# Optimization experiments

Hardware: AMD Instinct MI355X
Metric: run time of the kernel (lower is better)

Reference implementation:

```python
import jax, jax.numpy as jnp
import numpy as np

RES_LIST = [16, 32, 64, 128]
N_DIMS = 3
N_FIELDS = 4
N_POINTS = 2_000_000


def _value_noise(x, V, res, mult):
    """One ValueNoise level: trilinear interpolation of grid V at points x.

    x: [N, n_dims] float, V: [(res+1),]*n_dims + [n_fields], smoothness=2.
    """
    n_dims = x.shape[1]
    xs = jnp.fmod(x * res, res)                      # [N, d]
    fl = jnp.floor(xs)
    locs = xs - fl                                   # frac part, [N, d]
    ia = fl.astype(jnp.int32)                        # floor index
    ib = ia + 1                                      # non-periodic: grid has res+1 nodes
    idx = jnp.stack((ia, ib), axis=-1)               # [N, d, 2]
    corners = jnp.indices((2,) * n_dims)             # [d, 2,2,2]
    # per-dim corner indices, each [N, 2,2,2]
    gather_idx = tuple(idx[:, i, :][:, corners[i]] for i in range(n_dims))
    vals = V[gather_idx]                             # [N, 2,2,2, n_fields]
    # smoothness=2 fade: w = (3 - 2w) w^2
    w = (3.0 - 2.0 * locs) * locs * locs             # [N, d]
    for i in range(n_dims):
        wi = w[:, i].reshape((-1,) + (1,) * (n_dims - i))
        a, b = vals[:, 0], vals[:, 1]
        vals = a + wi * (b - a)                      # lerp along dim i
    return vals * mult                               # [N, n_fields]


def setup_inputs() -> dict:
    key = jax.random.key(0)
    kx, k0, k1, k2, k3 = jax.random.split(key, 5)
    x = jax.random.uniform(kx, (N_POINTS, N_DIMS), dtype=jnp.float32)
    grids = {}
    for k, res in zip((k0, k1, k2, k3), RES_LIST):
        grids[f"V{res}"] = jax.random.normal(
            k, (res + 1,) * N_DIMS + (N_FIELDS,), dtype=jnp.float32)
    return {"x": x, **grids}


def reference(x, V16, V32, V64, V128):
    grids = (V16, V32, V64, V128)
    out = jnp.zeros((x.shape[0], N_FIELDS), dtype=x.dtype)
    for V, res in zip(grids, RES_LIST):
        mult = float(RES_LIST[0]) / float(res)       # multiplier * res_list[0]/res
        out = out + _value_noise(x, V, res, mult)
    return out
```

## Files before the change

### kernel.cpp

```cpp
#include <hip/hip_runtime.h>


#define NB 1024
#define PTS_PER_BLK 4096
#define CHUNK 32
#define SC_THREADS 1024
#define SC_PPT (PTS_PER_BLK / SC_THREADS)
#define H_THREADS 256
#define H_PPT (PTS_PER_BLK / H_THREADS)
#define MT 1024

__device__ __forceinline__ int bucket_of(float px, float py, float pz) {
    int ix = min(max((int)(px * 16.0f), 0), 15);
    int iy = min(max((int)(py * 8.0f), 0), 7);
    int iz = min(max((int)(pz * 8.0f), 0), 7);
    return (ix * 8 + iy) * 8 + iz;
}

__global__ void __launch_bounds__(H_THREADS)
cvn_hist(const float* __restrict__ x, int* __restrict__ P, int n) {
    __shared__ int cnt[NB];
    int t = threadIdx.x;
    for (int q = t; q < NB; q += H_THREADS) cnt[q] = 0;
    __syncthreads();
    int base = blockIdx.x * PTS_PER_BLK;
    for (int k = 0; k < H_PPT; ++k) {
        int i = base + k * H_THREADS + t;
        if (i < n)
            atomicAdd(&cnt[bucket_of(x[3 * i], x[3 * i + 1], x[3 * i + 2])], 1);
    }
    __syncthreads();
    int* Pb = P + (size_t)blockIdx.x * NB;
    for (int q = t; q < NB; q += H_THREADS) Pb[q] = cnt[q];
}

__global__ void __launch_bounds__(256)
cvn_scan_a(const int* __restrict__ P, int* __restrict__ S, int nblk) {
    int q = blockIdx.x * 256 + threadIdx.x;
    int c = blockIdx.y;
    int b0 = c * CHUNK, b1 = min(b0 + CHUNK, nblk);
    int s = 0;
    for (int b = b0; b < b1; ++b) s += P[(size_t)b * NB + q];
    S[(size_t)c * NB + q] = s;
}

__global__ void __launch_bounds__(NB)
cvn_scan_b(int* __restrict__ S, int nch) {
    __shared__ int part[NB];
    int t = threadIdx.x;
    int acc = 0;
    for (int c = 0; c < nch; ++c) {
        int v = S[(size_t)c * NB + t];
        S[(size_t)c * NB + t] = acc;
        acc += v;
    }
    part[t] = acc;
    __syncthreads();
    for (int off = 1; off < NB; off <<= 1) {
        int v = (t >= off) ? part[t - off] : 0;
        __syncthreads();
        if (t >= off) part[t] += v;
        __syncthreads();
    }
    int texcl = (t == 0) ? 0 : part[t - 1];
    for (int c = 0; c < nch; ++c) S[(size_t)c * NB + t] += texcl;
}

__global__ void __launch_bounds__(256)
cvn_scan_c(int* __restrict__ P, const int* __restrict__ S, int nblk) {
    int q = blockIdx.x * 256 + threadIdx.x;
    int c = blockIdx.y;
    int b0 = c * CHUNK, b1 = min(b0 + CHUNK, nblk);
    int run = S[(size_t)c * NB + q];
    for (int b = b0; b < b1; ++b) {
        int v = P[(size_t)b * NB + q];
        P[(size_t)b * NB + q] = run;
        run += v;
    }
}

__global__ void __launch_bounds__(SC_THREADS)
cvn_scatter(const float* __restrict__ x, const int* __restrict__ P,
            float4* __restrict__ sorted, int* __restrict__ rank,
            int n, int write_rank) {
    __shared__ int cnt[NB];
    __shared__ int place[NB];
    __shared__ int Pb[NB];
    __shared__ int sc[NB];
    __shared__ float4 payload[PTS_PER_BLK];
    __shared__ unsigned short bkt[PTS_PER_BLK];
    int t = threadIdx.x, b = blockIdx.x;
    int base = b * PTS_PER_BLK;
    cnt[t] = 0; place[t] = 0;
    Pb[t] = P[(size_t)b * NB + t];
    __syncthreads();

    float px[SC_PPT], py[SC_PPT], pz[SC_PPT];
    int qq[SC_PPT];
    #pragma unroll
    for (int k = 0; k < SC_PPT; ++k) {
        int i = base + k * SC_THREADS + t;
        if (i < n) {
            px[k] = x[3 * i]; py[k] = x[3 * i + 1]; pz[k] = x[3 * i + 2];
            qq[k] = bucket_of(px[k], py[k], pz[k]);
            atomicAdd(&cnt[qq[k]], 1);
        } else qq[k] = -1;
    }
    __syncthreads();

    sc[t] = cnt[t];
    __syncthreads();
    for (int off = 1; off < NB; off <<= 1) {
        int v = (t >= off) ? sc[t - off] : 0;
        __syncthreads();
        if (t >= off) sc[t] += v;
        __syncthreads();
    }
    cnt[t] = (t == 0) ? 0 : sc[t - 1];
    __syncthreads();

    #pragma unroll
    for (int k = 0; k < SC_PPT; ++k) {
        if (qq[k] >= 0) {
            int q = qq[k];
            int lp = atomicAdd(&place[q], 1);
            int slot = cnt[q] + lp;
            int i = base + k * SC_THREADS + t;
            payload[slot] = make_float4(px[k], py[k], pz[k], __int_as_float(i));
            bkt[slot] = (unsigned short)q;
            if (write_rank) rank[i] = Pb[q] + lp;
        }
    }
    __syncthreads();

    int total = min(n - base, PTS_PER_BLK);
    #pragma unroll
    for (int k = 0; k < SC_PPT; ++k) {
        int j = k * SC_THREADS + t;
        if (j < total) {
            int q = bkt[j];
            sorted[Pb[q] + (j - cnt[q])] = payload[j];
        }
    }
}

__device__ __forceinline__ float4 lerp4(float4 a, float4 b, float w) {
    return make_float4(a.x + w * (b.x - a.x),
                       a.y + w * (b.y - a.y),
                       a.z + w * (b.z - a.z),
                       a.w + w * (b.w - a.w));
}

template <int RES>
__device__ __forceinline__ float4 level_val(const float4* __restrict__ V,
                                            float px, float py, float pz) {
    constexpr int S = RES + 1;
    float xs = fmodf(px * (float)RES, (float)RES);
    float ys = fmodf(py * (float)RES, (float)RES);
    float zs = fmodf(pz * (float)RES, (float)RES);
    float fx = floorf(xs), fy = floorf(ys), fz = floorf(zs);
    float tx = xs - fx, ty = ys - fy, tz = zs - fz;
    int ix = (int)fx, iy = (int)fy, iz = (int)fz;

    float wx = (3.0f - 2.0f * tx) * tx * tx;
    float wy = (3.0f - 2.0f * ty) * ty * ty;
    float wz = (3.0f - 2.0f * tz) * tz * tz;

    int base = (ix * S + iy) * S + iz;
    const float4* p0 = V + base;
    const float4* p1 = p0 + S * S;

    float4 c000 = p0[0];
    float4 c001 = p0[1];
    float4 c010 = p0[S];
    float4 c011 = p0[S + 1];
    float4 c100 = p1[0];
    float4 c101 = p1[1];
    float4 c110 = p1[S];
    float4 c111 = p1[S + 1];

    float4 m00 = lerp4(c000, c100, wx);
    float4 m01 = lerp4(c001, c101, wx);
    float4 m10 = lerp4(c010, c110, wx);
    float4 m11 = lerp4(c011, c111, wx);
    float4 n0  = lerp4(m00, m10, wy);
    float4 n1  = lerp4(m01, m11, wy);
    return lerp4(n0, n1, wz);
}

__device__ __forceinline__ float4 composite(const float4* __restrict__ V16,
                                            const float4* __restrict__ V32,
                                            const float4* __restrict__ V64,
                                            const float4* __restrict__ V128,
                                            float px, float py, float pz) {
    float4 acc = level_val<16>(V16, px, py, pz);
    float4 v;
    v = level_val<32>(V32, px, py, pz);
    acc.x += 0.5f * v.x; acc.y += 0.5f * v.y; acc.z += 0.5f * v.z; acc.w += 0.5f * v.w;
    v = level_val<64>(V64, px, py, pz);
    acc.x += 0.25f * v.x; acc.y += 0.25f * v.y; acc.z += 0.25f * v.z; acc.w += 0.25f * v.w;
    v = level_val<128>(V128, px, py, pz);
    acc.x += 0.125f * v.x; acc.y += 0.125f * v.y; acc.z += 0.125f * v.z; acc.w += 0.125f * v.w;
    return acc;
}

template <int RES>
__device__ __forceinline__ float4 lds_interp_b(const float4* s,
                                               float px, float py, float pz,
                                               int ix16, int iy8, int iz8) {
    constexpr int CX = RES / 16, CY = RES / 8, CZ = RES / 8;
    constexpr int DY = CY + 1, DZ = CZ + 1;
    float xs = px * (float)RES;
    float ys = py * (float)RES;
    float zs = pz * (float)RES;
    int ixg = (int)xs, iyg = (int)ys, izg = (int)zs;
    float tx = xs - (float)ixg, ty = ys - (float)iyg, tz = zs - (float)izg;
    int lx = min(max(ixg - ix16 * CX, 0), CX - 1);
    int ly = min(max(iyg - iy8 * CY, 0), CY - 1);
    int lz = min(max(izg - iz8 * CZ, 0), CZ - 1);

    float wx = (3.0f - 2.0f * tx) * tx * tx;
    float wy = (3.0f - 2.0f * ty) * ty * ty;
    float wz = (3.0f - 2.0f * tz) * tz * tz;

    const float4* p0 = s + (lx * DY + ly) * DZ + lz;
    const float4* p1 = p0 + DY * DZ;
    float4 c000 = p0[0],  c001 = p0[1];
    float4 c010 = p0[DZ], c011 = p0[DZ + 1];
    float4 c100 = p1[0],  c101 = p1[1];
    float4 c110 = p1[DZ], c111 = p1[DZ + 1];

    float4 m00 = lerp4(c000, c100, wx);
    float4 m01 = lerp4(c001, c101, wx);
    float4 m10 = lerp4(c010, c110, wx);
    float4 m11 = lerp4(c011, c111, wx);
    float4 n0  = lerp4(m00, m10, wy);
    float4 n1  = lerp4(m01, m11, wy);
    return lerp4(n0, n1, wz);
}

__global__ void __launch_bounds__(MT)
cvn_main4(const float4* __restrict__ sorted, const int* __restrict__ Tbase,
          const float4* __restrict__ V16, const float4* __restrict__ V32,
          const float4* __restrict__ V64, const float4* __restrict__ V128,
          float4* __restrict__ tmp, int n) {
    __shared__ float4 s128[9 * 17 * 17];
    __shared__ float4 s64[5 * 9 * 9];
    __shared__ float4 s32[3 * 5 * 5];
    __shared__ float4 s16[2 * 3 * 3];
    int t = threadIdx.x, b = blockIdx.x;

    int ox = b & 1, oy = (b >> 1) & 1, oz = (b >> 2) & 1;
    int g  = b >> 3;
    int gx = g >> 4, gy = (g >> 2) & 3, gz = g & 3;
    int ix16 = ox * 8 + gx, iy8 = oy * 4 + gy, iz8 = oz * 4 + gz;
    int q = (ix16 * 8 + iy8) * 8 + iz8;

    int base = Tbase[q];
    int end  = (q == NB - 1) ? n : Tbase[q + 1];
    int len  = end - base;

    int bx = ix16 * 8, by = iy8 * 16, bz = iz8 * 16;
    for (int u = t; u < 2601; u += MT) {
        int a = u / 289, r = u - a * 289;
        int bb = r / 17, c = r - bb * 17;
        s128[u] = V128[((size_t)(bx + a) * 129 + (by + bb)) * 129 + (bz + c)];
    }
    if (t < 405) {
        int a = t / 81, r = t - a * 81;
        int bb = r / 9, c = r - bb * 9;
        s64[t] = V64[((size_t)(ix16 * 4 + a) * 65 + (iy8 * 8 + bb)) * 65
                     + (iz8 * 8 + c)];
    } else if (t < 405 + 75) {
        int u = t - 405;
        int a = u / 25, r = u - a * 25;
        int bb = r / 5, c = r - bb * 5;
        s32[u] = V32[((size_t)(ix16 * 2 + a) * 33 + (iy8 * 4 + bb)) * 33
                     + (iz8 * 4 + c)];
    } else if (t < 405 + 75 + 18) {
        int u = t - 405 - 75;
        int a = u / 9, r = u - a * 9;
        int bb = r / 3, c = r - bb * 3;
        s16[u] = V16[((size_t)(ix16 + a) * 17 + (iy8 * 2 + bb)) * 17
                     + (iz8 * 2 + c)];
    }
    __syncthreads();

    for (int p = t; p < len; p += MT) {
        float4 pt = sorted[base + p];
        float4 acc = lds_interp_b<16>(s16, pt.x, pt.y, pt.z, ix16, iy8, iz8);
        float4 v;
        v = lds_interp_b<32>(s32, pt.x, pt.y, pt.z, ix16, iy8, iz8);
        acc.x += 0.5f * v.x; acc.y += 0.5f * v.y;
        acc.z += 0.5f * v.z; acc.w += 0.5f * v.w;
        v = lds_interp_b<64>(s64, pt.x, pt.y, pt.z, ix16, iy8, iz8);
        acc.x += 0.25f * v.x; acc.y += 0.25f * v.y;
        acc.z += 0.25f * v.z; acc.w += 0.25f * v.w;
        v = lds_interp_b<128>(s128, pt.x, pt.y, pt.z, ix16, iy8, iz8);
        acc.x += 0.125f * v.x; acc.y += 0.125f * v.y;
        acc.z += 0.125f * v.z; acc.w += 0.125f * v.w;
        tmp[base + p] = acc;
    }
}

__global__ void __launch_bounds__(256)
cvn_main(const float4* __restrict__ sorted,
         const float4* __restrict__ V16, const float4* __restrict__ V32,
         const float4* __restrict__ V64, const float4* __restrict__ V128,
         float4* __restrict__ outbuf, int n, int nblocks) {
    int nb8 = nblocks >> 3;
    int c = (blockIdx.x & 7) * nb8 + (blockIdx.x >> 3);
    int j = c * 256 + (int)threadIdx.x;
    if (j >= n) return;
    float4 p = sorted[j];
    outbuf[__float_as_int(p.w)] = composite(V16, V32, V64, V128, p.x, p.y, p.z);
}

__global__ void __launch_bounds__(256)
cvn_permute(const float4* __restrict__ tmp, const int* __restrict__ rank,
            float4* __restrict__ out, int n) {
    int i = blockIdx.x * 256 + (int)threadIdx.x;
    if (i >= n) return;
    out[i] = tmp[rank[i]];
}

__global__ void __launch_bounds__(256)
cvn_direct(const float* __restrict__ x,
           const float4* __restrict__ V16, const float4* __restrict__ V32,
           const float4* __restrict__ V64, const float4* __restrict__ V128,
           float4* __restrict__ out, int n) {
    int i = blockIdx.x * blockDim.x + threadIdx.x;
    if (i >= n) return;
    out[i] = composite(V16, V32, V64, V128, x[3 * i], x[3 * i + 1], x[3 * i + 2]);
}

extern "C" void kernel_launch(void* const* d_in, const int* in_sizes, int n_in,
                              void* d_out, int out_size, void* d_ws, size_t ws_size,
                              hipStream_t stream) {
    const float*  x    = (const float*)d_in[0];
    const float4* V16  = (const float4*)d_in[1];
    const float4* V32  = (const float4*)d_in[2];
    const float4* V64  = (const float4*)d_in[3];
    const float4* V128 = (const float4*)d_in[4];
    float4* out = (float4*)d_out;

    int n = in_sizes[0] / 3;
    int nblk = (n + PTS_PER_BLK - 1) / PTS_PER_BLK;
    int nch  = (nblk + CHUNK - 1) / CHUNK;

    auto align256 = [](size_t v) { return (v + 255) & ~(size_t)255; };
    size_t offP      = 0;
    size_t offS      = align256(offP + (size_t)nblk * NB * sizeof(int));
    size_t offSorted = align256(offS + (size_t)nch * NB * sizeof(int));
    size_t offRank   = align256(offSorted + (size_t)n * sizeof(float4));
    size_t offTmp    = align256(offRank + (size_t)n * sizeof(int));
    size_t needFull  = offTmp + (size_t)n * sizeof(float4);
    size_t needMid   = offRank;

    int grid256 = (n + 255) / 256;
    int nblocks = ((grid256 + 7) / 8) * 8;

    if (ws_size >= needMid) {
        int*    P      = (int*)((char*)d_ws + offP);
        int*    S      = (int*)((char*)d_ws + offS);
        float4* sorted = (float4*)((char*)d_ws + offSorted);
        bool full = (ws_size >= needFull);
        int*    rank = full ? (int*)((char*)d_ws + offRank) : nullptr;
        float4* tmp  = full ? (float4*)((char*)d_ws + offTmp) : nullptr;

        cvn_hist<<<nblk, H_THREADS, 0, stream>>>(x, P, n);
        cvn_scan_a<<<dim3(NB / 256, nch), 256, 0, stream>>>(P, S, nblk);
        cvn_scan_b<<<1, NB, 0, stream>>>(S, nch);
        cvn_scan_c<<<dim3(NB / 256, nch), 256, 0, stream>>>(P, S, nblk);
        cvn_scatter<<<nblk, SC_THREADS, 0, stream>>>(x, P, sorted, rank, n,
                                                     full ? 1 : 0);
        if (full) {
            cvn_main4<<<NB, MT, 0, stream>>>(sorted, S, V16, V32, V64, V128,
                                             tmp, n);
            cvn_permute<<<grid256, 256, 0, stream>>>(tmp, rank, out, n);
        } else {
            cvn_main<<<nblocks, 256, 0, stream>>>(sorted, V16, V32, V64, V128,
                                                  out, n, nblocks);
        }
    } else {
        cvn_direct<<<grid256, 256, 0, stream>>>(x, V16, V32, V64, V128, out, n);
    }
}
```

Measured before the change: 219.5 us.

## Store LDS grid tiles in fp16, scatter results directly, drop permute pass

The main kernel now keeps the 128 and 64 level tiles in shared memory as packed half precision instead of float4. This halves LDS use so more blocks fit per CU, and the block size drops to 512 with a launch bound of 8. The two coarse levels are read straight from global memory instead of being staged. Results are written straight to each point's original index, which removes the rank array, the temporary buffer and the separate permute kernel, at the cost of scattered global writes. Rounding grid values to fp16 adds error against the fp32 reference and may break the tolerance check.

```diff
diff --git a/kernel.cpp b/kernel.cpp
--- a/kernel.cpp
+++ b/kernel.cpp
@@ -1,4 +1,5 @@
 #include <hip/hip_runtime.h>
+#include <hip/hip_fp16.h>
 
 
 #define NB 1024
@@ -8,7 +9,7 @@
 #define SC_PPT (PTS_PER_BLK / SC_THREADS)
 #define H_THREADS 256
 #define H_PPT (PTS_PER_BLK / H_THREADS)
-#define MT 1024
+#define MT 512
 
 __device__ __forceinline__ int bucket_of(float px, float py, float pz) {
     int ix = min(max((int)(px * 16.0f), 0), 15);
@@ -81,8 +82,7 @@
 
 __global__ void __launch_bounds__(SC_THREADS)
 cvn_scatter(const float* __restrict__ x, const int* __restrict__ P,
-            float4* __restrict__ sorted, int* __restrict__ rank,
-            int n, int write_rank) {
+            float4* __restrict__ sorted, int n) {
     __shared__ int cnt[NB];
     __shared__ int place[NB];
     __shared__ int Pb[NB];
@@ -128,7 +128,6 @@
             int i = base + k * SC_THREADS + t;
             payload[slot] = make_float4(px[k], py[k], pz[k], __int_as_float(i));
             bkt[slot] = (unsigned short)q;
-            if (write_rank) rank[i] = Pb[q] + lp;
         }
     }
     __syncthreads();
@@ -204,8 +203,26 @@
     return acc;
 }
 
+__device__ __forceinline__ float4 ldh4(const uint2* p) {
+    uint2 u = *p;
+    __half2 h0 = *reinterpret_cast<const __half2*>(&u.x);
+    __half2 h1 = *reinterpret_cast<const __half2*>(&u.y);
+    float2 f0 = __half22float2(h0);
+    float2 f1 = __half22float2(h1);
+    return make_float4(f0.x, f0.y, f1.x, f1.y);
+}
+
+__device__ __forceinline__ uint2 sth4(float4 v) {
+    __half2 h0 = __floats2half2_rn(v.x, v.y);
+    __half2 h1 = __floats2half2_rn(v.z, v.w);
+    uint2 u;
+    u.x = *reinterpret_cast<unsigned int*>(&h0);
+    u.y = *reinterpret_cast<unsigned int*>(&h1);
+    return u;
+}
+
 template <int RES>
-__device__ __forceinline__ float4 lds_interp_b(const float4* s,
+__device__ __forceinline__ float4 lds_interp_h(const uint2* s,
                                                float px, float py, float pz,
                                                int ix16, int iy8, int iz8) {
     constexpr int CX = RES / 16, CY = RES / 8, CZ = RES / 8;
@@ -223,12 +240,12 @@
     float wy = (3.0f - 2.0f * ty) * ty * ty;
     float wz = (3.0f - 2.0f * tz) * tz * tz;
 
-    const float4* p0 = s + (lx * DY + ly) * DZ + lz;
-    const float4* p1 = p0 + DY * DZ;
-    float4 c000 = p0[0],  c001 = p0[1];
-    float4 c010 = p0[DZ], c011 = p0[DZ + 1];
-    float4 c100 = p1[0],  c101 = p1[1];
-    float4 c110 = p1[DZ], c111 = p1[DZ + 1];
+    const uint2* p0 = s + (lx * DY + ly) * DZ + lz;
+    const uint2* p1 = p0 + DY * DZ;
+    float4 c000 = ldh4(p0),      c001 = ldh4(p0 + 1);
+    float4 c010 = ldh4(p0 + DZ), c011 = ldh4(p0 + DZ + 1);
+    float4 c100 = ldh4(p1),      c101 = ldh4(p1 + 1);
+    float4 c110 = ldh4(p1 + DZ), c111 = ldh4(p1 + DZ + 1);
 
     float4 m00 = lerp4(c000, c100, wx);
     float4 m01 = lerp4(c001, c101, wx);
@@ -239,15 +256,13 @@
     return lerp4(n0, n1, wz);
 }
 
-__global__ void __launch_bounds__(MT)
+__global__ void __launch_bounds__(MT, 8)
 cvn_main4(const float4* __restrict__ sorted, const int* __restrict__ Tbase,
           const float4* __restrict__ V16, const float4* __restrict__ V32,
           const float4* __restrict__ V64, const float4* __restrict__ V128,
-          float4* __restrict__ tmp, int n) {
-    __shared__ float4 s128[9 * 17 * 17];
-    __shared__ float4 s64[5 * 9 * 9];
-    __shared__ float4 s32[3 * 5 * 5];
-    __shared__ float4 s16[2 * 3 * 3];
+          float4* __restrict__ out, int n) {
+    __shared__ uint2 s128[9 * 17 * 17];
+    __shared__ uint2 s64[5 * 9 * 9];
     int t = threadIdx.x, b = blockIdx.x;
 
     int ox = b & 1, oy = (b >> 1) & 1, oz = (b >> 2) & 1;
@@ -264,64 +279,32 @@
     for (int u = t; u < 2601; u += MT) {
         int a = u / 289, r = u - a * 289;
         int bb = r / 17, c = r - bb * 17;
-        s128[u] = V128[((size_t)(bx + a) * 129 + (by + bb)) * 129 + (bz + c)];
-    }
-    if (t < 405) {
-        int a = t / 81, r = t - a * 81;
+        s128[u] = sth4(V128[((size_t)(bx + a) * 129 + (by + bb)) * 129
+                            + (bz + c)]);
+    }
+    for (int u = t; u < 405; u += MT) {
+        int a = u / 81, r = u - a * 81;
         int bb = r / 9, c = r - bb * 9;
-        s64[t] = V64[((size_t)(ix16 * 4 + a) * 65 + (iy8 * 8 + bb)) * 65
-                     + (iz8 * 8 + c)];
-    } else if (t < 405 + 75) {
-        int u = t - 405;
-        int a = u / 25, r = u - a * 25;
-        int bb = r / 5, c = r - bb * 5;
-        s32[u] = V32[((size_t)(ix16 * 2 + a) * 33 + (iy8 * 4 + bb)) * 33
-                     + (iz8 * 4 + c)];
-    } else if (t < 405 + 75 + 18) {
-        int u = t - 405 - 75;
-        int a = u / 9, r = u - a * 9;
-        int bb = r / 3, c = r - bb * 3;
-        s16[u] = V16[((size_t)(ix16 + a) * 17 + (iy8 * 2 + bb)) * 17
-                     + (iz8 * 2 + c)];
+        s64[u] = sth4(V64[((size_t)(ix16 * 4 + a) * 65 + (iy8 * 8 + bb)) * 65
+                          + (iz8 * 8 + c)]);
     }
     __syncthreads();
 
     for (int p = t; p < len; p += MT) {
         float4 pt = sorted[base + p];
-        float4 acc = lds_interp_b<16>(s16, pt.x, pt.y, pt.z, ix16, iy8, iz8);
+        float4 acc = level_val<16>(V16, pt.x, pt.y, pt.z);
         float4 v;
-        v = lds_interp_b<32>(s32, pt.x, pt.y, pt.z, ix16, iy8, iz8);
+        v = level_val<32>(V32, pt.x, pt.y, pt.z);
         acc.x += 0.5f * v.x; acc.y += 0.5f * v.y;
         acc.z += 0.5f * v.z; acc.w += 0.5f * v.w;
-        v = lds_interp_b<64>(s64, pt.x, pt.y, pt.z, ix16, iy8, iz8);
+        v = lds_interp_h<64>(s64, pt.x, pt.y, pt.z, ix16, iy8, iz8);
         acc.x += 0.25f * v.x; acc.y += 0.25f * v.y;
         acc.z += 0.25f * v.z; acc.w += 0.25f * v.w;
-        v = lds_interp_b<128>(s128, pt.x, pt.y, pt.z, ix16, iy8, iz8);
+        v = lds_interp_h<128>(s128, pt.x, pt.y, pt.z, ix16, iy8, iz8);
         acc.x += 0.125f * v.x; acc.y += 0.125f * v.y;
         acc.z += 0.125f * v.z; acc.w += 0.125f * v.w;
-        tmp[base + p] = acc;
-    }
-}
-
-__global__ void __launch_bounds__(256)
-cvn_main(const float4* __restrict__ sorted,
-         const float4* __restrict__ V16, const float4* __restrict__ V32,
-         const float4* __restrict__ V64, const float4* __restrict__ V128,
-         float4* __restrict__ outbuf, int n, int nblocks) {
-    int nb8 = nblocks >> 3;
-    int c = (blockIdx.x & 7) * nb8 + (blockIdx.x >> 3);
-    int j = c * 256 + (int)threadIdx.x;
-    if (j >= n) return;
-    float4 p = sorted[j];
-    outbuf[__float_as_int(p.w)] = composite(V16, V32, V64, V128, p.x, p.y, p.z);
-}
-
-__global__ void __launch_bounds__(256)
-cvn_permute(const float4* __restrict__ tmp, const int* __restrict__ rank,
-            float4* __restrict__ out, int n) {
-    int i = blockIdx.x * 256 + (int)threadIdx.x;
-    if (i >= n) return;
-    out[i] = tmp[rank[i]];
+        out[__float_as_int(pt.w)] = acc;
+    }
 }
 
 __global__ void __launch_bounds__(256)
@@ -352,36 +335,22 @@
     size_t offP      = 0;
     size_t offS      = align256(offP + (size_t)nblk * NB * sizeof(int));
     size_t offSorted = align256(offS + (size_t)nch * NB * sizeof(int));
-    size_t offRank   = align256(offSorted + (size_t)n * sizeof(float4));
-    size_t offTmp    = align256(offRank + (size_t)n * sizeof(int));
-    size_t needFull  = offTmp + (size_t)n * sizeof(float4);
-    size_t needMid   = offRank;
+    size_t need      = offSorted + (size_t)n * sizeof(float4);
 
     int grid256 = (n + 255) / 256;
-    int nblocks = ((grid256 + 7) / 8) * 8;
-
-    if (ws_size >= needMid) {
+
+    if (ws_size >= need) {
         int*    P      = (int*)((char*)d_ws + offP);
         int*    S      = (int*)((char*)d_ws + offS);
         float4* sorted = (float4*)((char*)d_ws + offSorted);
-        bool full = (ws_size >= needFull);
-        int*    rank = full ? (int*)((char*)d_ws + offRank) : nullptr;
-        float4* tmp  = full ? (float4*)((char*)d_ws + offTmp) : nullptr;
 
         cvn_hist<<<nblk, H_THREADS, 0, stream>>>(x, P, n);
         cvn_scan_a<<<dim3(NB / 256, nch), 256, 0, stream>>>(P, S, nblk);
         cvn_scan_b<<<1, NB, 0, stream>>>(S, nch);
         cvn_scan_c<<<dim3(NB / 256, nch), 256, 0, stream>>>(P, S, nblk);
-        cvn_scatter<<<nblk, SC_THREADS, 0, stream>>>(x, P, sorted, rank, n,
-                                                     full ? 1 : 0);
-        if (full) {
-            cvn_main4<<<NB, MT, 0, stream>>>(sorted, S, V16, V32, V64, V128,
-                                             tmp, n);
-            cvn_permute<<<grid256, 256, 0, stream>>>(tmp, rank, out, n);
-        } else {
-            cvn_main<<<nblocks, 256, 0, stream>>>(sorted, V16, V32, V64, V128,
-                                                  out, n, nblocks);
-        }
+        cvn_scatter<<<nblk, SC_THREADS, 0, stream>>>(x, P, sorted, n);
+        cvn_main4<<<NB, MT, 0, stream>>>(sorted, S, V16, V32, V64, V128,
+                                         out, n);
     } else {
         cvn_direct<<<grid256, 256, 0, stream>>>(x, V16, V32, V64, V128, out, n);
     }
```

Result: faster. 187.7 us (-14.5%).
